# Optimization experiments

Measured on AMD Instinct MI355X. Metric: run time of the kernel, lower is better.

Reference implementation:

```python
import jax, jax.numpy as jnp
import numpy as np

EPS = 1e-5
H = 16  # num_heads

def layer_norm(x, g, b):
    mu = jnp.mean(x, axis=-1, keepdims=True)
    var = jnp.mean(jnp.square(x - mu), axis=-1, keepdims=True)
    return (x - mu) * jax.lax.rsqrt(var + EPS) * g + b

def setup_inputs() -> dict:
    key = jax.random.key(0)
    ks = jax.random.split(key, 12)
    B, N, D, F = 4, 1024, 1024, 4096
    s = 0.02
    return {
        'x': jax.random.normal(ks[0], (B, N, D), jnp.float32),
        'ln1_g': jnp.ones((D,), jnp.float32), 'ln1_b': jnp.zeros((D,), jnp.float32),
        'Wq': s * jax.random.normal(ks[1], (D, D), jnp.float32), 'bq': jnp.zeros((D,), jnp.float32),
        'Wk': s * jax.random.normal(ks[2], (D, D), jnp.float32), 'bk': jnp.zeros((D,), jnp.float32),
        'Wv': s * jax.random.normal(ks[3], (D, D), jnp.float32), 'bv': jnp.zeros((D,), jnp.float32),
        'Wo': s * jax.random.normal(ks[4], (D, D), jnp.float32), 'bo': jnp.zeros((D,), jnp.float32),
        'ln2_g': jnp.ones((D,), jnp.float32), 'ln2_b': jnp.zeros((D,), jnp.float32),
        'W1': s * jax.random.normal(ks[5], (D, F), jnp.float32), 'b1': jnp.zeros((F,), jnp.float32),
        'W2': s * jax.random.normal(ks[6], (F, D), jnp.float32), 'b2': jnp.zeros((D,), jnp.float32),
        'pad_mask': jnp.zeros((B, N), jnp.bool_),
    }

def reference(x, ln1_g, ln1_b, Wq, bq, Wk, bk, Wv, bv, Wo, bo,
              ln2_g, ln2_b, W1, b1, W2, b2, pad_mask):
    B, N, D = x.shape
    c = D // H  # per-head channels
    h = layer_norm(x, ln1_g, ln1_b)
    q = (h @ Wq + bq).reshape(B, N, H, c).transpose(0, 2, 1, 3)  # b h n c
    k = (h @ Wk + bk).reshape(B, N, H, c).transpose(0, 2, 1, 3)
    v = (h @ Wv + bv).reshape(B, N, H, c).transpose(0, 2, 1, 3)
    q = q * (c ** -0.5)
    attn = jnp.einsum('bhic,bhjc->bhij', q, k)
    neg = -jnp.finfo(attn.dtype).max
    attn = jnp.where(pad_mask[:, None, None, :], neg, attn)
    causal = jnp.triu(jnp.ones((N, N), jnp.bool_), k=1)  # right-aligned, i==j
    attn = jnp.where(causal, neg, attn)
    attn = jax.nn.softmax(attn, axis=-1)
    o = jnp.einsum('bhij,bhjc->bhic', attn, v)
    o = o.transpose(0, 2, 1, 3).reshape(B, N, D)
    x = o @ Wo + bo + x  # attention residual
    m = layer_norm(x, ln2_g, ln2_b)
    m = jax.nn.gelu(m @ W1 + b1, approximate=False) @ W2 + b2
    return x + m
```

## Files before the change

### kernel.cpp

```cpp
#include <hip/hip_runtime.h>
#include <hip/hip_bf16.h>
#include <cmath>

typedef __bf16 bf16_t;
typedef __bf16 bf16x8 __attribute__((ext_vector_type(8)));
typedef __bf16 bf16x4 __attribute__((ext_vector_type(4)));
typedef float f32x4 __attribute__((ext_vector_type(4)));

#define AS1 __attribute__((address_space(1)))
#define AS3 __attribute__((address_space(3)))

__device__ __forceinline__ void async_lds16(const void* g, void* s) {
    __builtin_amdgcn_global_load_lds((const AS1 void*)g, (AS3 void*)s, 16, 0, 0);
}

__device__ __forceinline__ float bf2f(bf16_t v) { return (float)v; }

__device__ __forceinline__ void tile_coords(int gx, int gy, int& mb, int& nb) {
    const int nwg = gx * gy;
    int lin = blockIdx.y * gx + blockIdx.x;
    if ((nwg & 7) == 0) lin = (lin & 7) * (nwg >> 3) + (lin >> 3);
    if ((gx & 3) == 0 && (gy & 3) == 0) {
        const int st = lin >> 4, pos = lin & 15;
        const int stn = gx >> 2;
        mb = (st / stn) * 4 + (pos >> 2);
        nb = (st % stn) * 4 + (pos & 3);
    } else {
        mb = lin / gx; nb = lin % gx;
    }
}

__global__ __launch_bounds__(256) void k_transpose_bf16(
    const float* __restrict__ src, bf16_t* __restrict__ dst, int R, int C) {
    __shared__ float tile[32][33];
    const int tx = threadIdx.x & 31, ty = threadIdx.x >> 5;
    const int r0 = blockIdx.y << 5, c0 = blockIdx.x << 5;
#pragma unroll
    for (int i = 0; i < 32; i += 8)
        tile[ty + i][tx] = src[(size_t)(r0 + ty + i) * C + c0 + tx];
    __syncthreads();
#pragma unroll
    for (int i = 0; i < 32; i += 8)
        dst[(size_t)(c0 + ty + i) * R + r0 + tx] = (bf16_t)tile[tx][ty + i];
}

__global__ __launch_bounds__(256) void k_layernorm(
    const float* __restrict__ x, const float* __restrict__ g,
    const float* __restrict__ b, bf16_t* __restrict__ out) {
    const int row = blockIdx.x;
    const int t = threadIdx.x;
    const float4 xv = reinterpret_cast<const float4*>(x + (size_t)row * 1024)[t];
    float s = xv.x + xv.y + xv.z + xv.w;
    float s2 = xv.x * xv.x + xv.y * xv.y + xv.z * xv.z + xv.w * xv.w;
#pragma unroll
    for (int mk = 32; mk >= 1; mk >>= 1) {
        s += __shfl_xor(s, mk);
        s2 += __shfl_xor(s2, mk);
    }
    __shared__ float red[8];
    const int w = t >> 6, l = t & 63;
    if (l == 0) { red[w] = s; red[4 + w] = s2; }
    __syncthreads();
    s = red[0] + red[1] + red[2] + red[3];
    s2 = red[4] + red[5] + red[6] + red[7];
    const float mu = s * (1.0f / 1024.0f);
    const float var = s2 * (1.0f / 1024.0f) - mu * mu;
    const float rs = rsqrtf(var + 1e-5f);
    const float4 gv = reinterpret_cast<const float4*>(g)[t];
    const float4 bv = reinterpret_cast<const float4*>(b)[t];
    bf16x4 o4;
    o4[0] = (bf16_t)((xv.x - mu) * rs * gv.x + bv.x);
    o4[1] = (bf16_t)((xv.y - mu) * rs * gv.y + bv.y);
    o4[2] = (bf16_t)((xv.z - mu) * rs * gv.z + bv.z);
    o4[3] = (bf16_t)((xv.w - mu) * rs * gv.w + bv.w);
    *reinterpret_cast<bf16x4*>(out + (size_t)row * 1024 + t * 4) = o4;
}

__global__ __launch_bounds__(256) void k_reduce_ln4(
    const bf16_t* __restrict__ pp,
    const float* __restrict__ bo, const float* __restrict__ x,
    const float* __restrict__ g, const float* __restrict__ b,
    float* __restrict__ x2, bf16_t* __restrict__ m2, long long zs) {
    const int row = blockIdx.x;
    const int t = threadIdx.x;
    const size_t off = (size_t)row * 1024 + t * 4;
    const float4 bb = reinterpret_cast<const float4*>(bo)[t];
    const float4 xv = *reinterpret_cast<const float4*>(x + off);
    float4 v;
    v.x = bb.x + xv.x; v.y = bb.y + xv.y; v.z = bb.z + xv.z; v.w = bb.w + xv.w;
#pragma unroll
    for (int z = 0; z < 4; z++) {
        const bf16x4 p = *reinterpret_cast<const bf16x4*>(pp + z * zs + off);
        v.x += bf2f(p[0]); v.y += bf2f(p[1]); v.z += bf2f(p[2]); v.w += bf2f(p[3]);
    }
    *reinterpret_cast<float4*>(x2 + off) = v;
    float s = v.x + v.y + v.z + v.w;
    float s2 = v.x * v.x + v.y * v.y + v.z * v.z + v.w * v.w;
#pragma unroll
    for (int mk = 32; mk >= 1; mk >>= 1) {
        s += __shfl_xor(s, mk);
        s2 += __shfl_xor(s2, mk);
    }
    __shared__ float red[8];
    const int w = t >> 6, l = t & 63;
    if (l == 0) { red[w] = s; red[4 + w] = s2; }
    __syncthreads();
    s = red[0] + red[1] + red[2] + red[3];
    s2 = red[4] + red[5] + red[6] + red[7];
    const float mu = s * (1.0f / 1024.0f);
    const float var = s2 * (1.0f / 1024.0f) - mu * mu;
    const float rs = rsqrtf(var + 1e-5f);
    const float4 gv = reinterpret_cast<const float4*>(g)[t];
    const float4 bv = reinterpret_cast<const float4*>(b)[t];
    bf16x4 o4;
    o4[0] = (bf16_t)((v.x - mu) * rs * gv.x + bv.x);
    o4[1] = (bf16_t)((v.y - mu) * rs * gv.y + bv.y);
    o4[2] = (bf16_t)((v.z - mu) * rs * gv.z + bv.z);
    o4[3] = (bf16_t)((v.w - mu) * rs * gv.w + bv.w);
    *reinterpret_cast<bf16x4*>(m2 + off) = o4;
}

__global__ __launch_bounds__(256) void k_reduce_out4(
    const bf16_t* __restrict__ pA, const bf16_t* __restrict__ pB,
    const float* __restrict__ b2, const float* __restrict__ x2,
    float* __restrict__ outp, long long zs) {
    const size_t off = ((size_t)blockIdx.x * 256 + threadIdx.x) * 4;
    const float4 c = *reinterpret_cast<const float4*>(x2 + off);
    const float4 bi = reinterpret_cast<const float4*>(b2)[(off >> 2) & 255];
    float4 v;
    v.x = c.x + bi.x; v.y = c.y + bi.y; v.z = c.z + bi.z; v.w = c.w + bi.w;
#pragma unroll
    for (int z = 0; z < 2; z++) {
        const bf16x4 a = *reinterpret_cast<const bf16x4*>(pA + z * zs + off);
        const bf16x4 b = *reinterpret_cast<const bf16x4*>(pB + z * zs + off);
        v.x += bf2f(a[0]) + bf2f(b[0]);
        v.y += bf2f(a[1]) + bf2f(b[1]);
        v.z += bf2f(a[2]) + bf2f(b[2]);
        v.w += bf2f(a[3]) + bf2f(b[3]);
    }
    *reinterpret_cast<float4*>(outp + off) = v;
}

enum { EPI_QKV = 0, EPI_GELU = 1, EPI_PARTB = 2 };

template <int EPI>
__global__ __launch_bounds__(256, 3) void k_gemm2(
    const bf16_t* __restrict__ A, const bf16_t* __restrict__ BT,
    const float* __restrict__ bias0, const float* __restrict__ bias1,
    const float* __restrict__ bias2,
    bf16_t* __restrict__ outB, bf16_t* __restrict__ outB2,
    bf16_t* __restrict__ outB3,
    int M, int N, int Ksub, int Kstr, long long zstride) {
    int mb, nb;
    tile_coords(gridDim.x, gridDim.y, mb, nb);
    const int mbase = mb * 128;
    const int nbase = nb * 128;

    const bf16_t* Ab = A + (size_t)blockIdx.z * Ksub;
    const bf16_t* Bb = BT + (size_t)blockIdx.z * Ksub;

    const int t = threadIdx.x;
    const int w = t >> 6, l = t & 63;
    const int wr = w >> 1, wc = w & 1;
    const int lrow = l & 15, lg = l >> 4;

    __shared__ alignas(16) bf16_t As[3][128 * 32];
    __shared__ alignas(16) bf16_t Bs[3][128 * 32];

    f32x4 acc[4][4] = {};

    const int sr = t >> 2;
    const int sc = t & 3;
    const int ssw = (sc ^ ((sr >> 1) & 3)) * 8;

    auto stage = [&](int ks, int buf) {
        const int k0 = ks << 5;
#pragma unroll
        for (int c = 0; c < 2; c++)
            async_lds16(Ab + (size_t)(mbase + c * 64 + sr) * Kstr + k0 + ssw,
                        &As[buf][c * 2048 + t * 8]);
#pragma unroll
        for (int c = 0; c < 2; c++)
            async_lds16(Bb + (size_t)(nbase + c * 64 + sr) * Kstr + k0 + ssw,
                        &Bs[buf][c * 2048 + t * 8]);
    };

    stage(0, 0);
    stage(1, 1);
    const int nt = Ksub >> 5;
    int cur = 0;
    for (int tt = 0; tt < nt; tt++) {
        asm volatile("s_waitcnt vmcnt(4)" ::: "memory");
        __builtin_amdgcn_sched_barrier(0);
        __builtin_amdgcn_s_barrier();
        __builtin_amdgcn_sched_barrier(0);
        if (tt + 2 < nt) {
            int nbuf = cur + 2; if (nbuf >= 3) nbuf -= 3;
            stage(tt + 2, nbuf);
        }
        bf16x8 a[4], b[4];
#pragma unroll
        for (int i = 0; i < 4; i++) {
            const int r = wr * 64 + i * 16 + lrow;
            a[i] = *reinterpret_cast<const bf16x8*>(
                &As[cur][r * 32 + ((lg ^ ((r >> 1) & 3)) * 8)]);
        }
#pragma unroll
        for (int j = 0; j < 4; j++) {
            const int r = wc * 64 + j * 16 + lrow;
            b[j] = *reinterpret_cast<const bf16x8*>(
                &Bs[cur][r * 32 + ((lg ^ ((r >> 1) & 3)) * 8)]);
        }
        __builtin_amdgcn_s_setprio(1);
#pragma unroll
        for (int i = 0; i < 4; i++)
#pragma unroll
            for (int j = 0; j < 4; j++)
                acc[i][j] = __builtin_amdgcn_mfma_f32_16x16x32_bf16(a[i], b[j], acc[i][j], 0, 0, 0);
        __builtin_amdgcn_s_setprio(0);
        cur = cur + 1; if (cur >= 3) cur = 0;
    }

#pragma unroll
    for (int i = 0; i < 4; i++) {
#pragma unroll
        for (int j = 0; j < 4; j++) {
            const int col = nbase + wc * 64 + j * 16 + lrow;
            float bj = 0.f;
            int kind = 0, cc = col;
            if constexpr (EPI == EPI_QKV) {
                kind = col >> 10; cc = col & 1023;
                bj = (kind == 0 ? bias0 : kind == 1 ? bias1 : bias2)[cc];
            } else if constexpr (EPI == EPI_GELU) {
                bj = bias0[col];
            }
#pragma unroll
            for (int r = 0; r < 4; r++) {
                const int row = mbase + wr * 64 + i * 16 + lg * 4 + r;
                const float v = acc[i][j][r] + bj;
                if constexpr (EPI == EPI_QKV) {
                    const int bidx = row >> 10, ns = row & 1023;
                    const int hh = cc >> 6, ch = cc & 63;
                    const int bhh = bidx * 16 + hh;
                    if (kind == 0)
                        outB[((size_t)bhh * 1024 + ns) * 64 + ch] = (bf16_t)(v * 0.125f);
                    else if (kind == 1)
                        outB2[((size_t)bhh * 1024 + ns) * 64 + ch] = (bf16_t)v;
                    else
                        outB3[((size_t)bhh * 64 + ch) * 1024 + ns] = (bf16_t)v;
                } else if constexpr (EPI == EPI_GELU) {
                    const float ge = 0.5f * v * (1.0f + erff(v * 0.70710678118654752f));
                    outB[(size_t)row * N + col] = (bf16_t)ge;
                } else {
                    bf16_t* po = (blockIdx.z < 2 ? outB : outB2) +
                                 (size_t)(blockIdx.z & 1) * zstride;
                    po[(size_t)row * N + col] = (bf16_t)v;
                }
            }
        }
    }
}

template <int EPI>
__global__ __launch_bounds__(512, 2) void k_gemm256(
    const bf16_t* __restrict__ A, const bf16_t* __restrict__ BT,
    const float* __restrict__ bias0,
    bf16_t* __restrict__ outB, bf16_t* __restrict__ outB2,
    int M, int N, int Ksub, int Kstr, long long zstride) {
    int mb, nb;
    tile_coords(gridDim.x, gridDim.y, mb, nb);
    const int mbase = mb * 256;
    const int nbase = nb * 256;

    const bf16_t* Ab = A + (size_t)blockIdx.z * Ksub;
    const bf16_t* Bb = BT + (size_t)blockIdx.z * Ksub;

    const int t = threadIdx.x;
    const int w = t >> 6, l = t & 63;
    const int wr = w >> 2, wc = w & 3;
    const int lrow = l & 15, lg = l >> 4;

    __shared__ alignas(16) bf16_t As[2][256 * 64];
    __shared__ alignas(16) bf16_t Bs[2][256 * 64];

    f32x4 acc[8][4] = {};

    const int sr = t >> 3;
    const int ssw = ((t & 7) ^ (sr & 7)) * 8;

    const bf16_t* pa = Ab + (size_t)(mbase + sr) * Kstr + ssw;
    const bf16_t* pb = Bb + (size_t)(nbase + sr) * Kstr + ssw;

    auto stage = [&](int kt, int buf) {
        const int k0 = kt << 6;
#pragma unroll
        for (int i = 0; i < 4; i++)
            async_lds16(pa + (size_t)(i * 64) * Kstr + k0, &As[buf][i * 4096 + t * 8]);
#pragma unroll
        for (int i = 0; i < 4; i++)
            async_lds16(pb + (size_t)(i * 64) * Kstr + k0, &Bs[buf][i * 4096 + t * 8]);
    };

    stage(0, 0);
    __syncthreads();
    const int nt = Ksub >> 6;
    for (int kt = 0; kt < nt; kt++) {
        const int cur = kt & 1;
        if (kt + 1 < nt) stage(kt + 1, cur ^ 1);
        bf16x8 bfr[4][2];
#pragma unroll
        for (int fj = 0; fj < 4; fj++) {
            const int rb = wc * 64 + fj * 16 + lrow;
#pragma unroll
            for (int ks = 0; ks < 2; ks++)
                bfr[fj][ks] = *reinterpret_cast<const bf16x8*>(
                    &Bs[cur][rb * 64 + (((ks * 4 + lg) ^ (rb & 7)) * 8)]);
        }
#pragma unroll
        for (int h = 0; h < 2; h++) {
            bf16x8 afr[4][2];
#pragma unroll
            for (int fi = 0; fi < 4; fi++) {
                const int ra = h * 128 + wr * 64 + fi * 16 + lrow;
#pragma unroll
                for (int ks = 0; ks < 2; ks++)
                    afr[fi][ks] = *reinterpret_cast<const bf16x8*>(
                        &As[cur][ra * 64 + (((ks * 4 + lg) ^ (ra & 7)) * 8)]);
            }
            __builtin_amdgcn_s_setprio(1);
#pragma unroll
            for (int fi = 0; fi < 4; fi++)
#pragma unroll
                for (int fj = 0; fj < 4; fj++)
#pragma unroll
                    for (int ks = 0; ks < 2; ks++)
                        acc[h * 4 + fi][fj] = __builtin_amdgcn_mfma_f32_16x16x32_bf16(
                            afr[fi][ks], bfr[fj][ks], acc[h * 4 + fi][fj], 0, 0, 0);
            __builtin_amdgcn_s_setprio(0);
        }
        __syncthreads();
    }

#pragma unroll
    for (int h = 0; h < 2; h++) {
#pragma unroll
        for (int fi = 0; fi < 4; fi++) {
#pragma unroll
            for (int fj = 0; fj < 4; fj++) {
                const int col = nbase + wc * 64 + fj * 16 + lrow;
                float bj = 0.f;
                if constexpr (EPI == EPI_GELU) bj = bias0[col];
#pragma unroll
                for (int r = 0; r < 4; r++) {
                    const int row = mbase + h * 128 + wr * 64 + fi * 16 + lg * 4 + r;
                    const float v = acc[h * 4 + fi][fj][r] + bj;
                    if constexpr (EPI == EPI_GELU) {
                        const float ge = 0.5f * v * (1.0f + erff(v * 0.70710678118654752f));
                        outB[(size_t)row * N + col] = (bf16_t)ge;
                    } else {
                        bf16_t* po = (blockIdx.z < 2 ? outB : outB2) +
                                     (size_t)(blockIdx.z & 1) * zstride;
                        po[(size_t)row * N + col] = (bf16_t)v;
                    }
                }
            }
        }
    }
}

__global__ __launch_bounds__(256, 4) void k_attn(
    const bf16_t* __restrict__ q, const bf16_t* __restrict__ kk,
    const bf16_t* __restrict__ vt, const unsigned char* __restrict__ pad,
    bf16_t* __restrict__ o) {
    const int qt = 15 - (blockIdx.x >> 6);
    const int bh = blockIdx.x & 63;
    const int bb = bh >> 4, hh = bh & 15;
    const int t = threadIdx.x;
    const int w = t >> 6, l = t & 63;
    const int lrow = l & 15, lg = l >> 4;
    const int qbase = qt * 64;

    __shared__ alignas(16) bf16_t Ks[64 * 64];
    __shared__ alignas(16) bf16_t Vs[64 * 64];
    __shared__ alignas(16) bf16_t Ps[4][16 * 64];

    const size_t bh_off = (size_t)bh * 1024 * 64;
    const int qrow = qbase + w * 16 + lrow;
    bf16x8 qf[2];
#pragma unroll
    for (int ks = 0; ks < 2; ks++)
        qf[ks] = *reinterpret_cast<const bf16x8*>(q + bh_off + (size_t)qrow * 64 + ks * 32 + lg * 8);

    f32x4 oacc[4] = {};
    float mrow[4] = {-1e30f, -1e30f, -1e30f, -1e30f};
    float lsum[4] = {0.f, 0.f, 0.f, 0.f};

    const int sr = t >> 3;
    const int ssw = ((t & 7) ^ (sr & 7)) * 8;

    for (int kb = 0; kb < qbase + 64; kb += 64) {
        __syncthreads();
        const bf16_t* kp = kk + bh_off + (size_t)kb * 64;
        async_lds16(kp + (size_t)sr * 64 + ssw, Ks + t * 8);
        async_lds16(kp + (size_t)(32 + sr) * 64 + ssw, Ks + 2048 + t * 8);
        const bf16_t* vp = vt + bh_off + kb;
        async_lds16(vp + (size_t)sr * 1024 + ssw, Vs + t * 8);
        async_lds16(vp + (size_t)(32 + sr) * 1024 + ssw, Vs + 2048 + t * 8);
        __syncthreads();

        f32x4 s[4] = {};
#pragma unroll
        for (int ks = 0; ks < 2; ks++) {
#pragma unroll
            for (int jt = 0; jt < 4; jt++) {
                const int kr = jt * 16 + lrow;
                bf16x8 bfr = *reinterpret_cast<const bf16x8*>(
                    Ks + kr * 64 + (((ks * 4 + lg) ^ (kr & 7)) * 8));
                s[jt] = __builtin_amdgcn_mfma_f32_16x16x32_bf16(qf[ks], bfr, s[jt], 0, 0, 0);
            }
        }
#pragma unroll
        for (int jt = 0; jt < 4; jt++) {
            const int kvg = kb + jt * 16 + lrow;
            const bool padm = pad[bb * 1024 + kvg] != 0;
#pragma unroll
            for (int r = 0; r < 4; r++) {
                const int qg = qbase + w * 16 + lg * 4 + r;
                if (kvg > qg || padm) s[jt][r] = -1e30f;
            }
        }
        float alpha[4];
#pragma unroll
        for (int r = 0; r < 4; r++) {
            float mx = fmaxf(fmaxf(s[0][r], s[1][r]), fmaxf(s[2][r], s[3][r]));
#pragma unroll
            for (int mk = 8; mk >= 1; mk >>= 1) mx = fmaxf(mx, __shfl_xor(mx, mk));
            const float mn = fmaxf(mrow[r], mx);
            alpha[r] = __expf(mrow[r] - mn);
            mrow[r] = mn;
        }
#pragma unroll
        for (int jt = 0; jt < 4; jt++)
#pragma unroll
            for (int r = 0; r < 4; r++)
                s[jt][r] = __expf(s[jt][r] - mrow[r]);
#pragma unroll
        for (int r = 0; r < 4; r++) {
            float sm = s[0][r] + s[1][r] + s[2][r] + s[3][r];
#pragma unroll
            for (int mk = 8; mk >= 1; mk >>= 1) sm += __shfl_xor(sm, mk);
            lsum[r] = lsum[r] * alpha[r] + sm;
        }
#pragma unroll
        for (int ct = 0; ct < 4; ct++)
#pragma unroll
            for (int r = 0; r < 4; r++)
                oacc[ct][r] *= alpha[r];
#pragma unroll
        for (int jt = 0; jt < 4; jt++)
#pragma unroll
            for (int r = 0; r < 4; r++) {
                const int prow = lg * 4 + r;
                const int kvc = jt * 16 + lrow;
                Ps[w][prow * 64 + (((kvc >> 3) ^ (prow & 7)) * 8) + (kvc & 7)] = (bf16_t)s[jt][r];
            }
#pragma unroll
        for (int ks = 0; ks < 2; ks++) {
            bf16x8 pa = *reinterpret_cast<const bf16x8*>(
                &Ps[w][lrow * 64 + (((ks * 4 + lg) ^ (lrow & 7)) * 8)]);
#pragma unroll
            for (int ct = 0; ct < 4; ct++) {
                const int vr = ct * 16 + lrow;
                bf16x8 vb = *reinterpret_cast<const bf16x8*>(
                    Vs + vr * 64 + (((ks * 4 + lg) ^ (vr & 7)) * 8));
                oacc[ct] = __builtin_amdgcn_mfma_f32_16x16x32_bf16(pa, vb, oacc[ct], 0, 0, 0);
            }
        }
    }
#pragma unroll
    for (int ct = 0; ct < 4; ct++) {
#pragma unroll
        for (int r = 0; r < 4; r++) {
            const int qg = qbase + w * 16 + lg * 4 + r;
            const float val = oacc[ct][r] / lsum[r];
            o[((size_t)bb * 1024 + qg) * 1024 + hh * 64 + ct * 16 + lrow] = (bf16_t)val;
        }
    }
}

extern "C" void kernel_launch(void* const* d_in, const int* in_sizes, int n_in,
                              void* d_out, int out_size, void* d_ws, size_t ws_size,
                              hipStream_t stream) {
    const float* x    = (const float*)d_in[0];
    const float* ln1g = (const float*)d_in[1];
    const float* ln1b = (const float*)d_in[2];
    const float* Wq   = (const float*)d_in[3];
    const float* bq   = (const float*)d_in[4];
    const float* Wk   = (const float*)d_in[5];
    const float* bk   = (const float*)d_in[6];
    const float* Wv   = (const float*)d_in[7];
    const float* bv   = (const float*)d_in[8];
    const float* Wo   = (const float*)d_in[9];
    const float* bo   = (const float*)d_in[10];
    const float* ln2g = (const float*)d_in[11];
    const float* ln2b = (const float*)d_in[12];
    const float* W1   = (const float*)d_in[13];
    const float* b1   = (const float*)d_in[14];
    const float* W2   = (const float*)d_in[15];
    const float* b2   = (const float*)d_in[16];
    const unsigned char* pad = (const unsigned char*)d_in[17];

    char* ws = (char*)d_ws;
    const size_t MB = 1024 * 1024;
    bf16_t* WqkvT = (bf16_t*)(ws + 0 * MB);
    bf16_t* WoT = (bf16_t*)(ws + 6 * MB);
    bf16_t* W1T = (bf16_t*)(ws + 8 * MB);
    bf16_t* W2T = (bf16_t*)(ws + 16 * MB);
    bf16_t* h   = (bf16_t*)(ws + 24 * MB);
    bf16_t* qb  = (bf16_t*)(ws + 32 * MB);
    bf16_t* kb  = (bf16_t*)(ws + 40 * MB);
    bf16_t* vb  = (bf16_t*)(ws + 48 * MB);
    bf16_t* ob  = (bf16_t*)(ws + 56 * MB);
    bf16_t* ppO = (bf16_t*)(ws + 24 * MB);
    bf16_t* m2  = (bf16_t*)(ws + 56 * MB);
    float*  x2  = (float*)(ws + 64 * MB);
    bf16_t* hid = (bf16_t*)(ws + 24 * MB);
    bf16_t* pW01 = (bf16_t*)(ws + 0 * MB);
    bf16_t* pW23 = (bf16_t*)(ws + 80 * MB);

    const long long ZS = 4ll * 1024 * 1024;

    const dim3 blk(256);
    const dim3 blk8(512);
    k_transpose_bf16<<<dim3(32, 32), blk, 0, stream>>>(Wq, WqkvT, 1024, 1024);
    k_transpose_bf16<<<dim3(32, 32), blk, 0, stream>>>(Wk, WqkvT + 1024 * 1024, 1024, 1024);
    k_transpose_bf16<<<dim3(32, 32), blk, 0, stream>>>(Wv, WqkvT + 2048 * 1024, 1024, 1024);
    k_transpose_bf16<<<dim3(32, 32), blk, 0, stream>>>(Wo, WoT, 1024, 1024);
    k_transpose_bf16<<<dim3(128, 32), blk, 0, stream>>>(W1, W1T, 1024, 4096);
    k_transpose_bf16<<<dim3(32, 128), blk, 0, stream>>>(W2, W2T, 4096, 1024);
    k_layernorm<<<4096, blk, 0, stream>>>(x, ln1g, ln1b, h);
    k_gemm2<EPI_QKV><<<dim3(24, 32), blk, 0, stream>>>(
        h, WqkvT, bq, bk, bv, qb, kb, vb, 4096, 3072, 1024, 1024, 0);
    k_attn<<<1024, blk, 0, stream>>>(qb, kb, vb, pad, ob);
    k_gemm2<EPI_PARTB><<<dim3(8, 32, 4), blk, 0, stream>>>(
        ob, WoT, nullptr, nullptr, nullptr, ppO, ppO + 2 * ZS, nullptr,
        4096, 1024, 256, 1024, ZS);
    k_reduce_ln4<<<4096, blk, 0, stream>>>(ppO, bo, x, ln2g, ln2b, x2, m2, ZS);
    k_gemm256<EPI_GELU><<<dim3(16, 16), blk8, 0, stream>>>(
        m2, W1T, b1, hid, nullptr, 4096, 4096, 1024, 1024, 0);
    k_gemm256<EPI_PARTB><<<dim3(4, 16, 4), blk8, 0, stream>>>(
        hid, W2T, nullptr, pW01, pW23, 4096, 1024, 1024, 4096, ZS);
    k_reduce_out4<<<4096, blk, 0, stream>>>(pW01, pW23, b2, x2, (float*)d_out, ZS);
}
```

Baseline: 241.4 us.

## Double-buffer attention K/V tiles, lazy softmax rescale, cache pad mask, merge transposes

The attention kernel now double-buffers K/V tiles in LDS, prefetching the next tile while computing the current one, with a single barrier per iteration. The pad mask is staged once into shared memory, and the online-softmax rescale runs only when a row max grows by more than 8, skipping the alpha multiplies otherwise. The six weight-transpose launches are merged into one kernel to cut launch overhead. Doubled LDS may lower occupancy, and the lazy rescale lets unnormalised values grow by up to e^8 in fp32/bf16.

```diff
diff --git a/kernel.cpp b/kernel.cpp
--- a/kernel.cpp
+++ b/kernel.cpp
@@ -30,18 +30,33 @@
     }
 }
 
-__global__ __launch_bounds__(256) void k_transpose_bf16(
-    const float* __restrict__ src, bf16_t* __restrict__ dst, int R, int C) {
-    __shared__ float tile[32][33];
+__global__ __launch_bounds__(256) void k_transpose_all(
+    const float* __restrict__ s0, const float* __restrict__ s1,
+    const float* __restrict__ s2, const float* __restrict__ s3,
+    const float* __restrict__ s4, const float* __restrict__ s5,
+    bf16_t* __restrict__ d0, bf16_t* __restrict__ d1, bf16_t* __restrict__ d2,
+    bf16_t* __restrict__ d3, bf16_t* __restrict__ d4, bf16_t* __restrict__ d5) {
+    const int b = blockIdx.x;
+    const float* src; bf16_t* dst; int R, C, gx, tile;
+    if (b < 4096) {
+        const int m = b >> 10; tile = b & 1023; gx = 32; R = 1024; C = 1024;
+        src = m == 0 ? s0 : m == 1 ? s1 : m == 2 ? s2 : s3;
+        dst = m == 0 ? d0 : m == 1 ? d1 : m == 2 ? d2 : d3;
+    } else if (b < 8192) {
+        tile = b - 4096; gx = 128; R = 1024; C = 4096; src = s4; dst = d4;
+    } else {
+        tile = b - 8192; gx = 32; R = 4096; C = 1024; src = s5; dst = d5;
+    }
+    const int r0 = (tile / gx) << 5, c0 = (tile % gx) << 5;
+    __shared__ float tl[32][33];
     const int tx = threadIdx.x & 31, ty = threadIdx.x >> 5;
-    const int r0 = blockIdx.y << 5, c0 = blockIdx.x << 5;
 #pragma unroll
     for (int i = 0; i < 32; i += 8)
-        tile[ty + i][tx] = src[(size_t)(r0 + ty + i) * C + c0 + tx];
+        tl[ty + i][tx] = src[(size_t)(r0 + ty + i) * C + c0 + tx];
     __syncthreads();
 #pragma unroll
     for (int i = 0; i < 32; i += 8)
-        dst[(size_t)(c0 + ty + i) * R + r0 + tx] = (bf16_t)tile[tx][ty + i];
+        dst[(size_t)(c0 + ty + i) * R + r0 + tx] = (bf16_t)tl[tx][ty + i];
 }
 
 __global__ __launch_bounds__(256) void k_layernorm(
@@ -380,11 +395,15 @@
     const int lrow = l & 15, lg = l >> 4;
     const int qbase = qt * 64;
 
-    __shared__ alignas(16) bf16_t Ks[64 * 64];
-    __shared__ alignas(16) bf16_t Vs[64 * 64];
+    __shared__ alignas(16) bf16_t Ks[2][64 * 64];
+    __shared__ alignas(16) bf16_t Vs[2][64 * 64];
     __shared__ alignas(16) bf16_t Ps[4][16 * 64];
+    __shared__ unsigned char padRow[1024];
 
     const size_t bh_off = (size_t)bh * 1024 * 64;
+    *reinterpret_cast<uchar4*>(&padRow[t * 4]) =
+        *reinterpret_cast<const uchar4*>(&pad[bb * 1024 + t * 4]);
+
     const int qrow = qbase + w * 16 + lrow;
     bf16x8 qf[2];
 #pragma unroll
@@ -398,15 +417,26 @@
     const int sr = t >> 3;
     const int ssw = ((t & 7) ^ (sr & 7)) * 8;
 
-    for (int kb = 0; kb < qbase + 64; kb += 64) {
-        __syncthreads();
+    auto stage = [&](int kb, int buf) {
         const bf16_t* kp = kk + bh_off + (size_t)kb * 64;
-        async_lds16(kp + (size_t)sr * 64 + ssw, Ks + t * 8);
-        async_lds16(kp + (size_t)(32 + sr) * 64 + ssw, Ks + 2048 + t * 8);
+        async_lds16(kp + (size_t)sr * 64 + ssw, &Ks[buf][t * 8]);
+        async_lds16(kp + (size_t)(32 + sr) * 64 + ssw, &Ks[buf][2048 + t * 8]);
         const bf16_t* vp = vt + bh_off + kb;
-        async_lds16(vp + (size_t)sr * 1024 + ssw, Vs + t * 8);
-        async_lds16(vp + (size_t)(32 + sr) * 1024 + ssw, Vs + 2048 + t * 8);
-        __syncthreads();
+        async_lds16(vp + (size_t)sr * 1024 + ssw, &Vs[buf][t * 8]);
+        async_lds16(vp + (size_t)(32 + sr) * 1024 + ssw, &Vs[buf][2048 + t * 8]);
+    };
+
+    stage(0, 0);
+    asm volatile("s_waitcnt lgkmcnt(0)" ::: "memory");
+    const int nkb = qt + 1;
+    for (int ib = 0; ib < nkb; ib++) {
+        const int cur = ib & 1;
+        const int kb = ib * 64;
+        asm volatile("s_waitcnt vmcnt(0)" ::: "memory");
+        __builtin_amdgcn_sched_barrier(0);
+        __builtin_amdgcn_s_barrier();
+        __builtin_amdgcn_sched_barrier(0);
+        if (ib + 1 < nkb) stage(kb + 64, cur ^ 1);
 
         f32x4 s[4] = {};
 #pragma unroll
@@ -415,29 +445,40 @@
             for (int jt = 0; jt < 4; jt++) {
                 const int kr = jt * 16 + lrow;
                 bf16x8 bfr = *reinterpret_cast<const bf16x8*>(
-                    Ks + kr * 64 + (((ks * 4 + lg) ^ (kr & 7)) * 8));
+                    &Ks[cur][kr * 64 + (((ks * 4 + lg) ^ (kr & 7)) * 8)]);
                 s[jt] = __builtin_amdgcn_mfma_f32_16x16x32_bf16(qf[ks], bfr, s[jt], 0, 0, 0);
             }
         }
 #pragma unroll
         for (int jt = 0; jt < 4; jt++) {
             const int kvg = kb + jt * 16 + lrow;
-            const bool padm = pad[bb * 1024 + kvg] != 0;
+            const bool padm = padRow[kvg] != 0;
 #pragma unroll
             for (int r = 0; r < 4; r++) {
                 const int qg = qbase + w * 16 + lg * 4 + r;
                 if (kvg > qg || padm) s[jt][r] = -1e30f;
             }
         }
-        float alpha[4];
+        float mx[4];
 #pragma unroll
         for (int r = 0; r < 4; r++) {
-            float mx = fmaxf(fmaxf(s[0][r], s[1][r]), fmaxf(s[2][r], s[3][r]));
-#pragma unroll
-            for (int mk = 8; mk >= 1; mk >>= 1) mx = fmaxf(mx, __shfl_xor(mx, mk));
-            const float mn = fmaxf(mrow[r], mx);
-            alpha[r] = __expf(mrow[r] - mn);
-            mrow[r] = mn;
+            float m0 = fmaxf(fmaxf(s[0][r], s[1][r]), fmaxf(s[2][r], s[3][r]));
+#pragma unroll
+            for (int mk = 8; mk >= 1; mk >>= 1) m0 = fmaxf(m0, __shfl_xor(m0, mk));
+            mx[r] = m0;
+        }
+        const bool need = (mx[0] > mrow[0] + 8.f) || (mx[1] > mrow[1] + 8.f) ||
+                          (mx[2] > mrow[2] + 8.f) || (mx[3] > mrow[3] + 8.f);
+        if (__any(need)) {
+#pragma unroll
+            for (int r = 0; r < 4; r++) {
+                const float mn = fmaxf(mrow[r], mx[r]);
+                const float al = __expf(mrow[r] - mn);
+                mrow[r] = mn;
+                lsum[r] *= al;
+#pragma unroll
+                for (int ct = 0; ct < 4; ct++) oacc[ct][r] *= al;
+            }
         }
 #pragma unroll
         for (int jt = 0; jt < 4; jt++)
@@ -449,13 +490,8 @@
             float sm = s[0][r] + s[1][r] + s[2][r] + s[3][r];
 #pragma unroll
             for (int mk = 8; mk >= 1; mk >>= 1) sm += __shfl_xor(sm, mk);
-            lsum[r] = lsum[r] * alpha[r] + sm;
-        }
-#pragma unroll
-        for (int ct = 0; ct < 4; ct++)
-#pragma unroll
-            for (int r = 0; r < 4; r++)
-                oacc[ct][r] *= alpha[r];
+            lsum[r] += sm;
+        }
 #pragma unroll
         for (int jt = 0; jt < 4; jt++)
 #pragma unroll
@@ -472,7 +508,7 @@
             for (int ct = 0; ct < 4; ct++) {
                 const int vr = ct * 16 + lrow;
                 bf16x8 vb = *reinterpret_cast<const bf16x8*>(
-                    Vs + vr * 64 + (((ks * 4 + lg) ^ (vr & 7)) * 8));
+                    &Vs[cur][vr * 64 + (((ks * 4 + lg) ^ (vr & 7)) * 8)]);
                 oacc[ct] = __builtin_amdgcn_mfma_f32_16x16x32_bf16(pa, vb, oacc[ct], 0, 0, 0);
             }
         }
@@ -532,12 +568,9 @@
 
     const dim3 blk(256);
     const dim3 blk8(512);
-    k_transpose_bf16<<<dim3(32, 32), blk, 0, stream>>>(Wq, WqkvT, 1024, 1024);
-    k_transpose_bf16<<<dim3(32, 32), blk, 0, stream>>>(Wk, WqkvT + 1024 * 1024, 1024, 1024);
-    k_transpose_bf16<<<dim3(32, 32), blk, 0, stream>>>(Wv, WqkvT + 2048 * 1024, 1024, 1024);
-    k_transpose_bf16<<<dim3(32, 32), blk, 0, stream>>>(Wo, WoT, 1024, 1024);
-    k_transpose_bf16<<<dim3(128, 32), blk, 0, stream>>>(W1, W1T, 1024, 4096);
-    k_transpose_bf16<<<dim3(32, 128), blk, 0, stream>>>(W2, W2T, 4096, 1024);
+    k_transpose_all<<<12288, blk, 0, stream>>>(
+        Wq, Wk, Wv, Wo, W1, W2,
+        WqkvT, WqkvT + 1024 * 1024, WqkvT + 2048 * 1024, WoT, W1T, W2T);
     k_layernorm<<<4096, blk, 0, stream>>>(x, ln1g, ln1b, h);
     k_gemm2<EPI_QKV><<<dim3(24, 32), blk, 0, stream>>>(
         h, WqkvT, bq, bk, bv, qb, kb, vb, 4096, 3072, 1024, 1024, 0);
```

Measured after the change: 229.1 us. -5.1%, faster.
